# Optimization experiments

Measured on AMD Instinct MI355X. Metric: run time of the kernel, lower is better.

The kernel has to match this reference:

```python
import jax, jax.numpy as jnp
import numpy as np

B, N, M = 4, 1024, 100
NB = 25
NTYPE = 2
TYPES = (1, 8)
FEAT = NB * NTYPE  # 50
H = 100
PI = 3.1415926
RMIN, RMAX = 0.5, 6.0


def setup_inputs() -> dict:
    key = jax.random.key(0)
    ks = jax.random.split(key, 12)
    type_map = jnp.array(TYPES)
    Imagetype = type_map[jax.random.randint(ks[0], (B, N), 0, NTYPE)]
    neighbor_list = jax.random.randint(ks[1], (B, N, M), 0, N + 1)
    rij = jax.random.uniform(ks[2], (B, N, M), minval=0.5, maxval=7.0)
    d = jax.random.normal(ks[3], (B, N, M, 3))
    d = d / jnp.linalg.norm(d, axis=-1, keepdims=True)
    ImagedR = jnp.concatenate([rij[..., None], d * rij[..., None]], axis=-1).astype(jnp.float32)

    def w(k, i, o):
        return (jax.random.normal(k, (NTYPE, i, o)) / np.sqrt(i + o)).astype(jnp.float32)

    def b(k, o):
        return jax.random.normal(k, (NTYPE, o)).astype(jnp.float32)

    return {"Imagetype": Imagetype, "neighbor_list": neighbor_list, "ImagedR": ImagedR,
            "W0": w(ks[4], FEAT, H), "b0": b(ks[5], H),
            "W1": w(ks[6], H, H), "b1": b(ks[7], H),
            "W2": w(ks[8], H, H), "b2": b(ks[9], H),
            "W3": w(ks[10], H, 1), "b3": b(ks[11], 1)}


def _net(x, W0, b0, W1, b1, W2, b2, W3, b3):
    # NET with network_size [50,100,100,100,1], tanh, resnet_dt=False
    h = jnp.tanh(x @ W0 + b0)
    x = h + jnp.concatenate([x, x], axis=-1)  # 50 -> 100 doubling skip
    h = jnp.tanh(x @ W1 + b1); x = h + x
    h = jnp.tanh(x @ W2 + b2); x = h + x
    return x @ W3 + b3


def _body2fun(Imagetype, neighbor_list, ImagedR):
    Bn, Nn, Mn = neighbor_list.shape
    rs = jnp.linspace(RMIN, RMAX, NB)  # [NB]
    r = ImagedR[..., 0]  # [B,N,M]
    rb = jnp.broadcast_to(r[..., None], (Bn, Nn, Mn, NB))

    def fc_fn(rt):
        env = jnp.exp(-(rt - rs) ** 2) * (0.5 * jnp.cos(PI * rt) + 0.5)
        return jnp.where((rt < RMAX) & (rt > 0), env, 0.0)

    # dfc = d(fc)/dr, elementwise, matching torch.autograd.grad with ones
    fc, dfc = jax.jvp(fc_fn, (rb,), (jnp.ones_like(rb),))

    # neighbor_type: 1-indexed lookup with 0 -> padding type 0
    padded = jnp.concatenate([jnp.zeros((Bn, 1), Imagetype.dtype), Imagetype], axis=1)
    nt = jnp.take_along_axis(padded, neighbor_list.reshape(Bn, -1), axis=1).reshape(Bn, Nn, Mn)

    dvec = jnp.where(r[..., None] != 0, ImagedR[..., 1:4] / r[..., None], 0.0)  # [B,N,M,3]

    feats, dfeats = [], []
    for t in TYPES:
        m = (nt == t)[..., None]  # [B,N,M,1]
        fct = jnp.where(m, fc, 0.0)
        dfct = jnp.where(m, dfc, 0.0)
        feats.append(fct.sum(axis=2))  # [B,N,NB]
        dfeats.append(dfct[..., None] * dvec[..., None, :])  # [B,N,M,NB,3]
    feat = jnp.concatenate(feats, axis=-1)  # [B,N,50]
    dfeat = jnp.concatenate(dfeats, axis=3)  # [B,N,M,50,3]
    return feat, dfeat


def reference(Imagetype, neighbor_list, ImagedR, W0, b0, W1, b1, W2, b2, W3, b3):
    Bn, Nn, Mn = neighbor_list.shape
    feat, dfeat = _body2fun(Imagetype, neighbor_list, ImagedR)

    type_arr = jnp.array(TYPES)
    mask = (Imagetype[None] == type_arr[:, None, None])[..., None]  # [T,B,N,1]

    def ei_fn(f):
        e = jax.vmap(_net, in_axes=(None, 0, 0, 0, 0, 0, 0, 0, 0))(
            f, W0, b0, W1, b1, W2, b2, W3, b3)  # [T,B,N,1]
        return jnp.sum(jnp.where(mask, e, 0.0), axis=0)  # [B,N,1]

    Ei = ei_fn(feat)
    Etot = jnp.sum(Ei, axis=1)  # [B,1]

    # dE/dfeat of total energy (grad_outputs = ones on Etot)
    dE = jax.grad(lambda f: jnp.sum(ei_fn(f)))(feat)  # [B,N,50]

    dE_Rid = jnp.einsum('bnf,bnmfc->bnmc', dE, dfeat)  # [B,N,M,3]
    Force = -dE_Rid.sum(axis=2)  # [B,N,3]

    # scatter-add of neighbor contributions: segment 0 is padding
    seg = jax.vmap(lambda v, i: jax.ops.segment_sum(v, i, num_segments=Nn + 1))(
        dE_Rid.reshape(Bn, -1, 3), neighbor_list.reshape(Bn, -1))  # [B,N+1,3]
    Force = Force + seg[:, 1:, :]
    return Etot, Ei, Force
```

## Files before the change

### kernel.cpp

```cpp
#include <hip/hip_runtime.h>

#define Bn   4
#define Nn   1024
#define Mn   100
#define NB   25
#define FEAT 50
#define PIc  3.1415926f
#define RSTEP (5.5f / 24.0f)

#define ATB  16
#define NATOMS (Bn * Nn)
#define NGPB  65
#define OBATCH (NGPB * ATB)
#define MF_BLOCKS (Bn * NGPB)
#define TYW  122880
#define PREP_BLKS 341
#define PSTRIDE ((Nn + 1) * 3)

typedef __attribute__((ext_vector_type(8))) short bf16x8;
typedef __attribute__((ext_vector_type(4))) float f32x4;

union U16x8 { unsigned short u[8]; bf16x8 v; uint4 q; };

__device__ __forceinline__ unsigned short f2bh(float x) {
    union { float f; unsigned u; } v; v.f = x;
    unsigned r = v.u + 0x7fffu + ((v.u >> 16) & 1u);
    return (unsigned short)(r >> 16);
}
__device__ __forceinline__ float bh2f(unsigned short h) {
    union { unsigned u; float f; } v; v.u = ((unsigned)h) << 16; return v.f;
}
__device__ __forceinline__ float fast_tanh(float x) {
    float ax = fabsf(x);
    float t  = __expf(-2.0f * ax);
    float r  = (1.0f - t) * __builtin_amdgcn_rcpf(1.0f + t);
    return copysignf(r, x);
}


__global__ __launch_bounds__(256) void stage1_kernel(
    const int* __restrict__ itype, const int* __restrict__ nlist,
    const float* __restrict__ dR,
    const float* __restrict__ W0, const float* __restrict__ W1,
    const float* __restrict__ W2,
    int* __restrict__ order, unsigned short* __restrict__ wsu,
    float* __restrict__ featp, float* __restrict__ Etot)
{
    const int blk = blockIdx.x;
    const int t = threadIdx.x;

    __shared__ float tile[64][65];
    __shared__ int scan[256];
    __shared__ float4 rc4[50];
    __shared__ float fpartial[64];

    if (blk < 20) {
        int ty = blk / 10, m = blk - ty * 10;
        int mat, jt, kt;
        if (m < 2)      { mat = 0; jt = m;            kt = 0; }
        else if (m < 6) { mat = 1; jt = (m - 2) >> 1; kt = (m - 2) & 1; }
        else            { mat = 2; jt = (m - 6) >> 1; kt = (m - 6) & 1; }
        const float* src = (mat == 0) ? W0 + ty * 5000
                          : (mat == 1) ? W1 + ty * 10000 : W2 + ty * 10000;
        const int Krows = (mat == 0) ? 50 : 100;
        const int Ck    = (mat == 0) ? 64 : 128;
        const int dH = ty * TYW + ((mat == 0) ? 0 : (mat == 1) ? 16384 : 49152);
        const int dL = dH + ((mat == 0) ? 8192 : 16384);
        const int j0 = jt * 64, k0 = kt * 64;
        const int rr0 = t >> 6, l = t & 63;
        #pragma unroll
        for (int i = 0; i < 16; ++i) {
            int rr = rr0 + 4 * i;
            int k = k0 + rr, j = j0 + l;
            tile[rr][l] = (k < Krows && j < 100) ? src[k * 100 + j] : 0.0f;
        }
        __syncthreads();
        #pragma unroll
        for (int i = 0; i < 16; ++i) {
            int jj = rr0 + 4 * i;
            float v = tile[l][jj];
            unsigned short h = f2bh(v);
            wsu[dH + (j0 + jj) * Ck + k0 + l] = h;
            wsu[dL + (j0 + jj) * Ck + k0 + l] = f2bh(v - bh2f(h));
        }
        return;
    }
    if (blk < 340) {
        int e = (blk - 20) * 256 + t;
        int ty = e / 40960;
        int r  = e - ty * 40960;
        float v = 0.0f; int dst;
        if (r < 16384) {
            int i = r >> 7, j = r & 127;
            if (i < 100 && j < 100) v = W2[ty * 10000 + i * 100 + j];
            dst = ty * TYW + 81920 + r;
        } else if (r < 32768) {
            int r2 = r - 16384; int i = r2 >> 7, j = r2 & 127;
            if (i < 100 && j < 100) v = W1[ty * 10000 + i * 100 + j];
            dst = ty * TYW + 98304 + r2;
        } else {
            int r2 = r - 32768; int f = r2 >> 7, j = r2 & 127;
            if (f < 50 && j < 100) v = W0[ty * 5000 + f * 100 + j];
            dst = ty * TYW + 114688 + r2;
        }
        wsu[dst] = f2bh(v);
        return;
    }
    if (blk == 340) {
        for (int i = t; i < Bn * OBATCH; i += 256) order[i] = -1;
        __syncthreads();
        for (int b = 0; b < Bn; ++b) {
            int tyv[4]; int c0 = 0;
            #pragma unroll
            for (int k = 0; k < 4; ++k) {
                int tt = (itype[b * Nn + t * 4 + k] == 8) ? 1 : 0;
                tyv[k] = tt; c0 += 1 - tt;
            }
            scan[t] = c0;
            __syncthreads();
            for (int off = 1; off < 256; off <<= 1) {
                int v = scan[t];
                int add = (t >= off) ? scan[t - off] : 0;
                __syncthreads();
                scan[t] = v + add;
                __syncthreads();
            }
            int total0 = scan[255];
            int ex0 = scan[t] - c0;
            int ex1 = 4 * t - ex0;
            int pad0 = (total0 + (ATB - 1)) & ~(ATB - 1);
            int p0 = ex0, p1 = pad0 + ex1;
            #pragma unroll
            for (int k = 0; k < 4; ++k) {
                int n = t * 4 + k;
                if (tyv[k] == 0) order[b * OBATCH + p0++] = n;
                else             order[b * OBATCH + p1++] = n;
            }
            __syncthreads();
        }
        if (t < Bn) Etot[t] = 0.0f;
        return;
    }

    const int atom = blk - PREP_BLKS;
    const int b = atom >> 10;

    if (t < Mn) {
        float4 qv = ((const float4*)dR)[(size_t)atom * Mn + t];
        float r = qv.x;
        int v = nlist[(size_t)atom * Mn + t];
        float cws = 0.0f;
        if (v > 0 && r > 0.0f && r < 6.0f) {
            float cw = 0.5f * __cosf(PIc * r) + 0.5f;
            cws = (itype[b * Nn + (v - 1)] == 8) ? -cw : cw;
        }
        ((float2*)rc4)[t] = make_float2(r, cws);
    }
    __syncthreads();

    float acc = 0.0f;
    if (t < 128) {
        const int w = t >> 6, l = t & 63;
        const int tt = l / NB;
        const float rk = 0.5f + (l - tt * NB) * RSTEP;
        #pragma unroll
        for (int i = 0; i < 25; ++i) {
            float4 pr = rc4[w * 25 + i];
            float d0 = pr.x - rk, d1 = pr.z - rk;
            float c0 = tt ? fmaxf(-pr.y, 0.0f) : fmaxf(pr.y, 0.0f);
            float c1 = tt ? fmaxf(-pr.w, 0.0f) : fmaxf(pr.w, 0.0f);
            acc += __expf(-d0 * d0) * c0 + __expf(-d1 * d1) * c1;
        }
        if (w == 1) fpartial[l] = acc;
    }
    __syncthreads();
    if (t < 64)
        featp[(size_t)atom * 64 + t] = (t < FEAT) ? (acc + fpartial[t]) : 0.0f;
}

#define ISSUE(RH, RL, OFFU, OFFL, RW, NKT, HASLO, COND)                       \
    if (COND) {                                                               \
        int jj_ = c + 16 * w;                                                 \
        _Pragma("unroll")                                                     \
        for (int kt = 0; kt < (NKT); ++kt) {                                  \
            int boff_ = jj_ * (RW) + kt * 32 + q * 8;                         \
            RH[kt] = *(const bf16x8*)(wb + (OFFU) + boff_);                   \
            if (HASLO) RL[kt] = *(const bf16x8*)(wb + (OFFL) + boff_);        \
        }                                                                     \
    }

#define GEMM_R(ABUF, RH, RL, NKT, HASLO)                                      \
    {                                                                         \
        acc = (f32x4){0,0,0,0}; accl = (f32x4){0,0,0,0};                      \
        _Pragma("unroll")                                                     \
        for (int kt = 0; kt < (NKT); ++kt) {                                  \
            int gk = kt * 4 + q;                                              \
            bf16x8 af = *(const bf16x8*)&aA[ABUF][(c << 7) | ((gk ^ (c & 7)) << 3)]; \
            acc = __builtin_amdgcn_mfma_f32_16x16x32_bf16(af, RH[kt], acc, 0, 0, 0); \
            if (HASLO) accl = __builtin_amdgcn_mfma_f32_16x16x32_bf16(af, RL[kt], accl, 0, 0, 0); \
        }                                                                     \
    }

#define WRACT(BUF, J, A, X)                                                   \
    aA[BUF][((A) << 7) | ((((J) >> 3) ^ ((A) & 7)) << 3) | ((J) & 7)] = f2bh(X)

__global__ __launch_bounds__(512) void mlpforce_kernel(
    const float* __restrict__ featp, const int* __restrict__ itype,
    const int* __restrict__ nlist, const float* __restrict__ dR,
    const int* __restrict__ order, const unsigned short* __restrict__ wsu,
    const float* __restrict__ B0, const float* __restrict__ B1,
    const float* __restrict__ B2, const float* __restrict__ W3,
    const float* __restrict__ B3,
    float* __restrict__ Ei, float* __restrict__ Etot,
    float* __restrict__ partial)
{
    const int t = threadIdx.x;
    const int w = t >> 6;
    const int lane = t & 63;
    const int c = lane & 15, q = lane >> 4;
    const int b = blockIdx.x / NGPB;
    const int grp = blockIdx.x - b * NGPB;

    __shared__ unsigned short aA[2][2048];
    __shared__ float fshf[16][52];
    __shared__ float dx1s[16][112];
    __shared__ float biasS[4][128];
    __shared__ float eip[8][16];
    __shared__ float eivals[16];
    __shared__ float deLDS[16][52];
    __shared__ float facc[PSTRIDE];
    __shared__ int aid[16];

    for (int idx = t; idx < PSTRIDE; idx += 512) facc[idx] = 0.0f;
    if (t < 16) aid[t] = order[b * OBATCH + grp * ATB + t];
    __syncthreads();

    int first = -1;
    #pragma unroll
    for (int a = 0; a < ATB; ++a) { int v = aid[a]; if (first < 0 && v >= 0) first = v; }

    if (first >= 0) {
        const int ty = (itype[b * Nn + first] == 8) ? 1 : 0;
        const unsigned short* wb = wsu + (size_t)ty * TYW;

        bf16x8 bh0[4], bl0[4], bh1[4], bl1[4];
        f32x4 acc, accl;
        float xr[4], h0r[4], h1r[4], h2r[4], dxr[4];

        ISSUE(bh0, bl0, 0, 8192, 64, 2, 1, true);
        if (t < 128) {
            const int srow = t >> 3, sg = t & 7;
            int v = aid[srow];
            float4 fa = {0,0,0,0}, fb = {0,0,0,0};
            if (v >= 0) {
                const float4* fp = (const float4*)(featp + ((size_t)(b * Nn + v)) * 64 + sg * 8);
                fa = fp[0]; fb = fp[1];
            }
            U16x8 pk;
            pk.u[0]=f2bh(fa.x); pk.u[1]=f2bh(fa.y); pk.u[2]=f2bh(fa.z); pk.u[3]=f2bh(fa.w);
            pk.u[4]=f2bh(fb.x); pk.u[5]=f2bh(fb.y); pk.u[6]=f2bh(fb.z); pk.u[7]=f2bh(fb.w);
            *(uint4*)&aA[0][(srow << 7) | ((sg ^ (srow & 7)) << 3)] = pk.q;
            int cbase = sg * 8;
            if (cbase < 52) {
                float vals[8] = {fa.x,fa.y,fa.z,fa.w,fb.x,fb.y,fb.z,fb.w};
                #pragma unroll
                for (int j7 = 0; j7 < 8; ++j7)
                    if (cbase + j7 < 52) fshf[srow][cbase + j7] = vals[j7];
            }
        }
        {
            int row = t >> 7, col = t & 127;
            const float* s = (row == 0) ? B0 : (row == 1) ? B1 : (row == 2) ? B2 : W3;
            biasS[row][col] = (col < 100) ? s[ty * 100 + col] : 0.0f;
        }
        __syncthreads();

        ISSUE(bh1, bl1, 16384, 32768, 128, 4, 1, true);
        GEMM_R(0, bh0, bl0, 2, 1);
        {
            int j = c + 16 * w;
            float bj = biasS[0][j];
            #pragma unroll
            for (int r = 0; r < 4; ++r) {
                int a = q * 4 + r;
                float z = acc[r] + accl[r] + bj;
                float h = 0.f, x = 0.f;
                if (j < 100) { h = fast_tanh(z); x = h + fshf[a][(j < 50) ? j : j - 50]; }
                h0r[r] = h; xr[r] = x;
                WRACT(1, j, a, x);
            }
        }
        __syncthreads();

        ISSUE(bh0, bl0, 49152, 65536, 128, 4, 1, true);
        GEMM_R(1, bh1, bl1, 4, 1);
        {
            int j = c + 16 * w;
            float bj = biasS[1][j];
            #pragma unroll
            for (int r = 0; r < 4; ++r) {
                int a = q * 4 + r;
                float z = acc[r] + accl[r] + bj;
                float h = (j < 100) ? fast_tanh(z) : 0.f;
                float x = (j < 100) ? (h + xr[r]) : 0.f;
                h1r[r] = h; xr[r] = x;
                WRACT(0, j, a, x);
            }
        }
        __syncthreads();

        ISSUE(bh1, bl1, 81920, 0, 128, 4, 0, true);
        GEMM_R(0, bh0, bl0, 4, 1);
        {
            int j = c + 16 * w;
            float bj = biasS[2][j];
            float wv = biasS[3][j];
            float p4v[4];
            #pragma unroll
            for (int r = 0; r < 4; ++r) {
                float z = acc[r] + accl[r] + bj;
                float h = (j < 100) ? fast_tanh(z) : 0.f;
                h2r[r] = h;
                xr[r] = (j < 100) ? (h + xr[r]) : 0.f;
                p4v[r] = xr[r] * wv;
            }
            #pragma unroll
            for (int off = 1; off < 16; off <<= 1) {
                #pragma unroll
                for (int r = 0; r < 4; ++r) p4v[r] += __shfl_xor(p4v[r], off);
            }
            if (c == 0) {
                #pragma unroll
                for (int r = 0; r < 4; ++r) eip[w][q * 4 + r] = p4v[r];
            }
            #pragma unroll
            for (int r = 0; r < 4; ++r) {
                int a = q * 4 + r;
                float d = wv * (1.0f - h2r[r] * h2r[r]);
                WRACT(1, j, a, d);
            }
        }
        __syncthreads();
        if (t < 16) {
            int v = aid[t];
            float e = 0.0f;
            if (v >= 0) {
                e = B3[ty];
                #pragma unroll
                for (int ww = 0; ww < 8; ++ww) e += eip[ww][t];
                Ei[b * Nn + v] = e;
            }
            eivals[t] = e;
        }

        ISSUE(bh0, bl0, 98304, 0, 128, 4, 0, true);
        GEMM_R(1, bh1, bl1, 4, 0);
        {
            int i = c + 16 * w;
            float w3i = biasS[3][i];
            #pragma unroll
            for (int r = 0; r < 4; ++r) {
                int a = q * 4 + r;
                float dx2 = acc[r] + w3i;
                dxr[r] = dx2;
                float d = dx2 * (1.0f - h1r[r] * h1r[r]);
                WRACT(0, i, a, d);
            }
        }
        __syncthreads();

        ISSUE(bh1, bl1, 114688, 0, 128, 4, 0, (w < 4));
        GEMM_R(0, bh0, bl0, 4, 0);
        {
            int i = c + 16 * w;
            #pragma unroll
            for (int r = 0; r < 4; ++r) {
                int a = q * 4 + r;
                float dx1 = dxr[r] + acc[r];
                if (i < 112) dx1s[a][i] = dx1;
                float d = dx1 * (1.0f - h0r[r] * h0r[r]);
                WRACT(1, i, a, d);
            }
        }
        __syncthreads();

        if (w < 4) {
            GEMM_R(1, bh1, bl1, 4, 0);
            int f = c + 16 * w;
            if (f < 50) {
                #pragma unroll
                for (int r = 0; r < 4; ++r) {
                    int a = q * 4 + r;
                    deLDS[a][f] = acc[r] + dx1s[a][f] + dx1s[a][f + 50];
                }
            }
        }
        __syncthreads();

        if (t == 0) {
            float s = 0.0f;
            #pragma unroll
            for (int i = 0; i < 16; ++i) s += eivals[i];
            atomicAdd(&Etot[b], s);
        }
        #pragma unroll
        for (int ai = 0; ai < 2; ++ai) {
            const int a = w * 2 + ai;
            const int n = aid[a];
            if (n >= 0) {
                const size_t pairbase = (size_t)(b * Nn + n) * Mn;
                const int m1 = lane + 64;
                float4 qv0 = ((const float4*)dR)[pairbase + lane];
                int    v0  = nlist[pairbase + lane];
                float4 qv1 = make_float4(0.f, 0.f, 0.f, 0.f);
                int    v1  = 0;
                if (m1 < Mn) {
                    qv1 = ((const float4*)dR)[pairbase + m1];
                    v1  = nlist[pairbase + m1];
                }
                float cfx = 0.f, cfy = 0.f, cfz = 0.f;
                #pragma unroll
                for (int mi = 0; mi < 2; ++mi) {
                    float4 qv = mi ? qv1 : qv0;
                    int v = mi ? v1 : v0;
                    if (v > 0) {
                        float r = qv.x;
                        if (r > 0.0f && r < 6.0f) {
                            int tt = (itype[b * Nn + v - 1] == 8) ? 1 : 0;
                            float cw  = 0.5f * __cosf(PIc * r) + 0.5f;
                            float dcw = -0.5f * PIc * __sinf(PIc * r);
                            float s = 0.0f;
                            const float* de = &deLDS[a][tt * NB];
                            #pragma unroll
                            for (int k = 0; k < NB; ++k) {
                                float d = r - (0.5f + k * RSTEP);
                                float e = __expf(-d * d);
                                s += de[k] * e * __builtin_fmaf(-2.0f * cw, d, dcw);
                            }
                            float inv = 1.0f / r;
                            float fx = s * qv.y * inv, fy = s * qv.z * inv, fz = s * qv.w * inv;
                            atomicAdd(&facc[v * 3 + 0], fx);
                            atomicAdd(&facc[v * 3 + 1], fy);
                            atomicAdd(&facc[v * 3 + 2], fz);
                            cfx += fx; cfy += fy; cfz += fz;
                        }
                    }
                }
                #pragma unroll
                for (int off = 32; off > 0; off >>= 1) {
                    cfx += __shfl_xor(cfx, off);
                    cfy += __shfl_xor(cfy, off);
                    cfz += __shfl_xor(cfz, off);
                }
                if (lane == 0) {
                    atomicAdd(&facc[(n + 1) * 3 + 0], -cfx);
                    atomicAdd(&facc[(n + 1) * 3 + 1], -cfy);
                    atomicAdd(&facc[(n + 1) * 3 + 2], -cfz);
                }
            }
        }
    }
    __syncthreads();

    float* pout = partial + (size_t)blockIdx.x * PSTRIDE;
    for (int idx = t; idx < PSTRIDE; idx += 512) pout[idx] = facc[idx];
}

__global__ __launch_bounds__(256) void freduce_kernel(
    const float* __restrict__ partial, float* __restrict__ Force)
{
    int idx = blockIdx.x * 256 + threadIdx.x;
    if (idx >= Bn * Nn * 3) return;
    int b = idx / (Nn * 3);
    int r = idx - b * (Nn * 3);
    int i = r / 3, ch = r - i * 3;
    float s = 0.0f;
    for (int g = 0; g < NGPB; ++g)
        s += partial[((size_t)(b * NGPB + g)) * PSTRIDE + (size_t)(i + 1) * 3 + ch];
    Force[idx] = s;
}

extern "C" void kernel_launch(void* const* d_in, const int* in_sizes, int n_in,
                              void* d_out, int out_size, void* d_ws, size_t ws_size,
                              hipStream_t stream)
{
    const int*   itype = (const int*)d_in[0];
    const int*   nlist = (const int*)d_in[1];
    const float* dR    = (const float*)d_in[2];
    const float* W0 = (const float*)d_in[3];  const float* B0 = (const float*)d_in[4];
    const float* W1 = (const float*)d_in[5];  const float* B1 = (const float*)d_in[6];
    const float* W2 = (const float*)d_in[7];  const float* B2 = (const float*)d_in[8];
    const float* W3 = (const float*)d_in[9];  const float* B3 = (const float*)d_in[10];

    float* out   = (float*)d_out;
    float* Etot  = out;
    float* Ei    = out + Bn;
    float* Force = out + Bn + Bn * Nn;

    float* featp   = (float*)d_ws;
    float* partial = featp + (size_t)NATOMS * 64;
    int*   order   = (int*)(partial + (size_t)MF_BLOCKS * PSTRIDE);
    unsigned short* wsu = (unsigned short*)(order + Bn * OBATCH);

    stage1_kernel  <<<PREP_BLKS + NATOMS, 256, 0, stream>>>(itype, nlist, dR,
                                                            W0, W1, W2,
                                                            order, wsu, featp, Etot);
    mlpforce_kernel<<<MF_BLOCKS, 512, 0, stream>>>(featp, itype, nlist, dR,
                                                   order, wsu,
                                                   B0, B1, B2, W3, B3,
                                                   Ei, Etot, partial);
    freduce_kernel <<<(Bn * Nn * 3 + 255) / 256, 256, 0, stream>>>(partial, Force);
}
```

Before: 52.67 us.

## Process 32 atoms per block, reusing weight fragments across two MFMA row tiles

Doubles the per-block atom batch from 16 to 32 and halves the number of blocks per batch. Each loaded weight fragment now feeds two MFMA row tiles, and each wave handles four atoms in the force stage. This halves the per-block partial-force buffers that the reduce kernel must sum. The cost is more registers and LDS per block and fewer blocks to spread across CUs, so occupancy and parallelism may drop.

```diff
diff --git a/kernel.cpp b/kernel.cpp
--- a/kernel.cpp
+++ b/kernel.cpp
@@ -8,9 +8,9 @@
 #define PIc  3.1415926f
 #define RSTEP (5.5f / 24.0f)
 
-#define ATB  16
+#define ATB  32
 #define NATOMS (Bn * Nn)
-#define NGPB  65
+#define NGPB  33
 #define OBATCH (NGPB * ATB)
 #define MF_BLOCKS (Bn * NGPB)
 #define TYW  122880
@@ -189,15 +189,22 @@
         }                                                                     \
     }
 
-#define GEMM_R(ABUF, RH, RL, NKT, HASLO)                                      \
+#define GEMM_R2(ABUF, RH, RL, NKT, HASLO)                                     \
     {                                                                         \
-        acc = (f32x4){0,0,0,0}; accl = (f32x4){0,0,0,0};                      \
+        acc[0] = (f32x4){0,0,0,0}; acc[1] = acc[0];                           \
+        accl[0] = acc[0]; accl[1] = acc[0];                                   \
         _Pragma("unroll")                                                     \
         for (int kt = 0; kt < (NKT); ++kt) {                                  \
             int gk = kt * 4 + q;                                              \
-            bf16x8 af = *(const bf16x8*)&aA[ABUF][(c << 7) | ((gk ^ (c & 7)) << 3)]; \
-            acc = __builtin_amdgcn_mfma_f32_16x16x32_bf16(af, RH[kt], acc, 0, 0, 0); \
-            if (HASLO) accl = __builtin_amdgcn_mfma_f32_16x16x32_bf16(af, RL[kt], accl, 0, 0, 0); \
+            int sw = ((gk ^ (c & 7)) << 3);                                   \
+            bf16x8 af0 = *(const bf16x8*)&aA[ABUF][(c << 7) | sw];            \
+            bf16x8 af1 = *(const bf16x8*)&aA[ABUF][((c + 16) << 7) | sw];     \
+            acc[0] = __builtin_amdgcn_mfma_f32_16x16x32_bf16(af0, RH[kt], acc[0], 0, 0, 0); \
+            acc[1] = __builtin_amdgcn_mfma_f32_16x16x32_bf16(af1, RH[kt], acc[1], 0, 0, 0); \
+            if (HASLO) {                                                      \
+                accl[0] = __builtin_amdgcn_mfma_f32_16x16x32_bf16(af0, RL[kt], accl[0], 0, 0, 0); \
+                accl[1] = __builtin_amdgcn_mfma_f32_16x16x32_bf16(af1, RL[kt], accl[1], 0, 0, 0); \
+            }                                                                 \
         }                                                                     \
     }
 
@@ -221,18 +228,18 @@
     const int b = blockIdx.x / NGPB;
     const int grp = blockIdx.x - b * NGPB;
 
-    __shared__ unsigned short aA[2][2048];
-    __shared__ float fshf[16][52];
-    __shared__ float dx1s[16][112];
+    __shared__ unsigned short aA[2][4096];
+    __shared__ float fshf[32][52];
+    __shared__ float dx1s[32][112];
     __shared__ float biasS[4][128];
-    __shared__ float eip[8][16];
-    __shared__ float eivals[16];
-    __shared__ float deLDS[16][52];
+    __shared__ float eip[8][32];
+    __shared__ float eivals[32];
+    __shared__ float deLDS[32][52];
     __shared__ float facc[PSTRIDE];
-    __shared__ int aid[16];
+    __shared__ int aid[32];
 
     for (int idx = t; idx < PSTRIDE; idx += 512) facc[idx] = 0.0f;
-    if (t < 16) aid[t] = order[b * OBATCH + grp * ATB + t];
+    if (t < 32) aid[t] = order[b * OBATCH + grp * ATB + t];
     __syncthreads();
 
     int first = -1;
@@ -244,11 +251,11 @@
         const unsigned short* wb = wsu + (size_t)ty * TYW;
 
         bf16x8 bh0[4], bl0[4], bh1[4], bl1[4];
-        f32x4 acc, accl;
-        float xr[4], h0r[4], h1r[4], h2r[4], dxr[4];
+        f32x4 acc[2], accl[2];
+        float xr[2][4], h0r[2][4], h1r[2][4], h2r[2][4], dxr[2][4];
 
         ISSUE(bh0, bl0, 0, 8192, 64, 2, 1, true);
-        if (t < 128) {
+        if (t < 256) {
             const int srow = t >> 3, sg = t & 7;
             int v = aid[srow];
             float4 fa = {0,0,0,0}, fb = {0,0,0,0};
@@ -276,72 +283,90 @@
         __syncthreads();
 
         ISSUE(bh1, bl1, 16384, 32768, 128, 4, 1, true);
-        GEMM_R(0, bh0, bl0, 2, 1);
+        GEMM_R2(0, bh0, bl0, 2, 1);
         {
             int j = c + 16 * w;
             float bj = biasS[0][j];
             #pragma unroll
-            for (int r = 0; r < 4; ++r) {
-                int a = q * 4 + r;
-                float z = acc[r] + accl[r] + bj;
-                float h = 0.f, x = 0.f;
-                if (j < 100) { h = fast_tanh(z); x = h + fshf[a][(j < 50) ? j : j - 50]; }
-                h0r[r] = h; xr[r] = x;
-                WRACT(1, j, a, x);
+            for (int rt = 0; rt < 2; ++rt) {
+                #pragma unroll
+                for (int r = 0; r < 4; ++r) {
+                    int a = rt * 16 + q * 4 + r;
+                    float z = acc[rt][r] + accl[rt][r] + bj;
+                    float h = 0.f, x = 0.f;
+                    if (j < 100) { h = fast_tanh(z); x = h + fshf[a][(j < 50) ? j : j - 50]; }
+                    h0r[rt][r] = h; xr[rt][r] = x;
+                    WRACT(1, j, a, x);
+                }
             }
         }
         __syncthreads();
 
         ISSUE(bh0, bl0, 49152, 65536, 128, 4, 1, true);
-        GEMM_R(1, bh1, bl1, 4, 1);
+        GEMM_R2(1, bh1, bl1, 4, 1);
         {
             int j = c + 16 * w;
             float bj = biasS[1][j];
             #pragma unroll
-            for (int r = 0; r < 4; ++r) {
-                int a = q * 4 + r;
-                float z = acc[r] + accl[r] + bj;
-                float h = (j < 100) ? fast_tanh(z) : 0.f;
-                float x = (j < 100) ? (h + xr[r]) : 0.f;
-                h1r[r] = h; xr[r] = x;
-                WRACT(0, j, a, x);
+            for (int rt = 0; rt < 2; ++rt) {
+                #pragma unroll
+                for (int r = 0; r < 4; ++r) {
+                    int a = rt * 16 + q * 4 + r;
+                    float z = acc[rt][r] + accl[rt][r] + bj;
+                    float h = (j < 100) ? fast_tanh(z) : 0.f;
+                    float x = (j < 100) ? (h + xr[rt][r]) : 0.f;
+                    h1r[rt][r] = h; xr[rt][r] = x;
+                    WRACT(0, j, a, x);
+                }
             }
         }
         __syncthreads();
 
         ISSUE(bh1, bl1, 81920, 0, 128, 4, 0, true);
-        GEMM_R(0, bh0, bl0, 4, 1);
+        GEMM_R2(0, bh0, bl0, 4, 1);
         {
             int j = c + 16 * w;
             float bj = biasS[2][j];
             float wv = biasS[3][j];
-            float p4v[4];
-            #pragma unroll
-            for (int r = 0; r < 4; ++r) {
-                float z = acc[r] + accl[r] + bj;
-                float h = (j < 100) ? fast_tanh(z) : 0.f;
-                h2r[r] = h;
-                xr[r] = (j < 100) ? (h + xr[r]) : 0.f;
-                p4v[r] = xr[r] * wv;
+            float p4v[2][4];
+            #pragma unroll
+            for (int rt = 0; rt < 2; ++rt) {
+                #pragma unroll
+                for (int r = 0; r < 4; ++r) {
+                    float z = acc[rt][r] + accl[rt][r] + bj;
+                    float h = (j < 100) ? fast_tanh(z) : 0.f;
+                    h2r[rt][r] = h;
+                    xr[rt][r] = (j < 100) ? (h + xr[rt][r]) : 0.f;
+                    p4v[rt][r] = xr[rt][r] * wv;
+                }
             }
             #pragma unroll
             for (int off = 1; off < 16; off <<= 1) {
                 #pragma unroll
-                for (int r = 0; r < 4; ++r) p4v[r] += __shfl_xor(p4v[r], off);
+                for (int rt = 0; rt < 2; ++rt) {
+                    #pragma unroll
+                    for (int r = 0; r < 4; ++r) p4v[rt][r] += __shfl_xor(p4v[rt][r], off);
+                }
             }
             if (c == 0) {
                 #pragma unroll
-                for (int r = 0; r < 4; ++r) eip[w][q * 4 + r] = p4v[r];
-            }
-            #pragma unroll
-            for (int r = 0; r < 4; ++r) {
-                int a = q * 4 + r;
-                float d = wv * (1.0f - h2r[r] * h2r[r]);
-                WRACT(1, j, a, d);
-            }
-        }
-        __syncthreads();
-        if (t < 16) {
+                for (int rt = 0; rt < 2; ++rt) {
+                    #pragma unroll
+                    for (int r = 0; r < 4; ++r) eip[w][rt * 16 + q * 4 + r] = p4v[rt][r];
+                }
+            }
+            #pragma unroll
+            for (int rt = 0; rt < 2; ++rt) {
+                #pragma unroll
+                for (int r = 0; r < 4; ++r) {
+                    int a = rt * 16 + q * 4 + r;
+                    float d = wv * (1.0f - h2r[rt][r] * h2r[rt][r]);
+                    WRACT(1, j, a, d);
+                }
+            }
+        }
+        __syncthreads();
+        if (t < 32) {
             int v = aid[t];
             float e = 0.0f;
             if (v >= 0) {
@@ -354,44 +379,53 @@
         }
 
         ISSUE(bh0, bl0, 98304, 0, 128, 4, 0, true);
-        GEMM_R(1, bh1, bl1, 4, 0);
+        GEMM_R2(1, bh1, bl1, 4, 0);
         {
             int i = c + 16 * w;
             float w3i = biasS[3][i];
             #pragma unroll
-            for (int r = 0; r < 4; ++r) {
-                int a = q * 4 + r;
-                float dx2 = acc[r] + w3i;
-                dxr[r] = dx2;
-                float d = dx2 * (1.0f - h1r[r] * h1r[r]);
-                WRACT(0, i, a, d);
+            for (int rt = 0; rt < 2; ++rt) {
+                #pragma unroll
+                for (int r = 0; r < 4; ++r) {
+                    int a = rt * 16 + q * 4 + r;
+                    float dx2 = acc[rt][r] + w3i;
+                    dxr[rt][r] = dx2;
+                    float d = dx2 * (1.0f - h1r[rt][r] * h1r[rt][r]);
+                    WRACT(0, i, a, d);
+                }
             }
         }
         __syncthreads();
 
         ISSUE(bh1, bl1, 114688, 0, 128, 4, 0, (w < 4));
-        GEMM_R(0, bh0, bl0, 4, 0);
+        GEMM_R2(0, bh0, bl0, 4, 0);
         {
             int i = c + 16 * w;
             #pragma unroll
-            for (int r = 0; r < 4; ++r) {
-                int a = q * 4 + r;
-                float dx1 = dxr[r] + acc[r];
-                if (i < 112) dx1s[a][i] = dx1;
-                float d = dx1 * (1.0f - h0r[r] * h0r[r]);
-                WRACT(1, i, a, d);
+            for (int rt = 0; rt < 2; ++rt) {
+                #pragma unroll
+                for (int r = 0; r < 4; ++r) {
+                    int a = rt * 16 + q * 4 + r;
+                    float dx1 = dxr[rt][r] + acc[rt][r];
+                    if (i < 112) dx1s[a][i] = dx1;
+                    float d = dx1 * (1.0f - h0r[rt][r] * h0r[rt][r]);
+                    WRACT(1, i, a, d);
+                }
             }
         }
         __syncthreads();
 
         if (w < 4) {
-            GEMM_R(1, bh1, bl1, 4, 0);
+            GEMM_R2(1, bh1, bl1, 4, 0);
             int f = c + 16 * w;
             if (f < 50) {
                 #pragma unroll
-                for (int r = 0; r < 4; ++r) {
-                    int a = q * 4 + r;
-                    deLDS[a][f] = acc[r] + dx1s[a][f] + dx1s[a][f + 50];
+                for (int rt = 0; rt < 2; ++rt) {
+                    #pragma unroll
+                    for (int r = 0; r < 4; ++r) {
+                        int a = rt * 16 + q * 4 + r;
+                        deLDS[a][f] = acc[rt][r] + dx1s[a][f] + dx1s[a][f + 50];
+                    }
                 }
             }
         }
@@ -400,12 +434,12 @@
         if (t == 0) {
             float s = 0.0f;
             #pragma unroll
-            for (int i = 0; i < 16; ++i) s += eivals[i];
+            for (int i = 0; i < 32; ++i) s += eivals[i];
             atomicAdd(&Etot[b], s);
         }
         #pragma unroll
-        for (int ai = 0; ai < 2; ++ai) {
-            const int a = w * 2 + ai;
+        for (int ai = 0; ai < 4; ++ai) {
+            const int a = w * 4 + ai;
             const int n = aid[a];
             if (n >= 0) {
                 const size_t pairbase = (size_t)(b * Nn + n) * Mn;
@@ -475,6 +509,7 @@
     int r = idx - b * (Nn * 3);
     int i = r / 3, ch = r - i * 3;
     float s = 0.0f;
+    #pragma unroll 8
     for (int g = 0; g < NGPB; ++g)
         s += partial[((size_t)(b * NGPB + g)) * PSTRIDE + (size_t)(i + 1) * 3 + ch];
     Force[idx] = s;
```

Result: faster. 49.95 us (-5.2%).
